# Performance work log

Measured on AMD Instinct MI355X. Metric: run time of the kernel, lower is better.

Reference implementation:

```python
import jax, jax.numpy as jnp
import numpy as np

N = 20000       # nodes
E = 320000      # edges (before self-loops)
F_IN = 128
HID = 128
HEADS = 4
OUT_DIM = 2
B = 64          # graphs in batch
SLOPE = 0.2     # GATv2 leaky_relu negative slope (PyG default)


def _glorot(key, shape):
    fan_in, fan_out = shape[0], shape[1]
    limit = np.sqrt(6.0 / (fan_in + fan_out)).astype(np.float32)
    return jax.random.uniform(key, shape, jnp.float32, -limit, limit)


def setup_inputs() -> dict:
    key = jax.random.key(0)
    ks = jax.random.split(key, 24)
    inp = {
        'x': jax.random.normal(ks[0], (N, F_IN), jnp.float32),
        'edge_src': jax.random.randint(ks[1], (E,), 0, N),
        'edge_dst': jax.random.randint(ks[2], (E,), 0, N),
        'batch': jnp.sort(jax.random.randint(ks[3], (N,), 0, B)),
        # layer 1: in=F_IN, out=HEADS*HID, concat
        'Wl1': _glorot(ks[4], (F_IN, HEADS * HID)),
        'Wr1': _glorot(ks[5], (F_IN, HEADS * HID)),
        'bl1': jnp.zeros((HEADS * HID,), jnp.float32),
        'br1': jnp.zeros((HEADS * HID,), jnp.float32),
        'att1': _glorot(ks[6], (HEADS, HID)),
        'bias1': jnp.zeros((HEADS * HID,), jnp.float32),
        # layer 2: in=HEADS*HID, out=HEADS*HID, concat
        'Wl2': _glorot(ks[7], (HEADS * HID, HEADS * HID)),
        'Wr2': _glorot(ks[8], (HEADS * HID, HEADS * HID)),
        'bl2': jnp.zeros((HEADS * HID,), jnp.float32),
        'br2': jnp.zeros((HEADS * HID,), jnp.float32),
        'att2': _glorot(ks[9], (HEADS, HID)),
        'bias2': jnp.zeros((HEADS * HID,), jnp.float32),
        # layer 3: in=HEADS*HID, heads=1, concat=False -> out=HID
        'Wl3': _glorot(ks[10], (HEADS * HID, HID)),
        'Wr3': _glorot(ks[11], (HEADS * HID, HID)),
        'bl3': jnp.zeros((HID,), jnp.float32),
        'br3': jnp.zeros((HID,), jnp.float32),
        'att3': _glorot(ks[12], (1, HID)),
        'bias3': jnp.zeros((HID,), jnp.float32),
        # output MLP
        'W_mlp1': _glorot(ks[13], (HID, HID)),
        'b_mlp1': jnp.zeros((HID,), jnp.float32),
        'W_mlp2': _glorot(ks[14], (HID, OUT_DIM)),
        'b_mlp2': jnp.zeros((OUT_DIM,), jnp.float32),
    }
    return inp


def gatv2_layer(x, src, dst, Wl, Wr, bl, br, att, bias, concat):
    """PyG GATv2Conv (eval mode): alpha_ij = softmax_j over N(i) of a^T LeakyReLU(xl_j + xr_i)."""
    H, C = att.shape
    n = x.shape[0]
    xl = (x @ Wl + bl).reshape(n, H, C)   # source transform
    e = jax.nn.leaky_relu(xl[src] + (x @ Wr + br).reshape(n, H, C)[dst], SLOPE)  # [E,H,C]
    logits = jnp.einsum('ehc,hc->eh', e, att)                                    # [E,H]
    # segment softmax over destination node
    m = jax.ops.segment_max(logits, dst, num_segments=n)
    alpha = jnp.exp(logits - m[dst])
    denom = jax.ops.segment_sum(alpha, dst, num_segments=n)
    alpha = alpha / denom[dst]
    out = jax.ops.segment_sum(xl[src] * alpha[..., None], dst, num_segments=n)   # [N,H,C]
    out = out.reshape(n, H * C) if concat else out.mean(axis=1)
    return out + bias


def reference(x, edge_src, edge_dst, batch,
              Wl1, Wr1, bl1, br1, att1, bias1,
              Wl2, Wr2, bl2, br2, att2, bias2,
              Wl3, Wr3, bl3, br3, att3, bias3,
              W_mlp1, b_mlp1, W_mlp2, b_mlp2):
    n = x.shape[0]
    loop = jnp.arange(n, dtype=edge_src.dtype)
    src = jnp.concatenate([edge_src, loop])   # PyG add_self_loops=True
    dst = jnp.concatenate([edge_dst, loop])

    h = jax.nn.elu(gatv2_layer(x, src, dst, Wl1, Wr1, bl1, br1, att1, bias1, True))
    h = jax.nn.elu(gatv2_layer(h, src, dst, Wl2, Wr2, bl2, br2, att2, bias2, True))
    h = jax.nn.elu(gatv2_layer(h, src, dst, Wl3, Wr3, bl3, br3, att3, bias3, False))

    # global_mean_pool over graph ids
    counts = jnp.maximum(jax.ops.segment_sum(jnp.ones((n,), h.dtype), batch, num_segments=B), 1.0)
    pooled = jax.ops.segment_sum(h, batch, num_segments=B) / counts[:, None]

    hidden = jax.nn.relu(pooled @ W_mlp1 + b_mlp1)
    return hidden @ W_mlp2 + b_mlp2
```

## Files before the change

### kernel.cpp

```cpp
#include <hip/hip_runtime.h>
#include <math.h>


typedef __attribute__((ext_vector_type(4))) float f32x4;
typedef __attribute__((ext_vector_type(8))) _Float16 f16x8;
typedef __attribute__((ext_vector_type(4))) _Float16 f16x4;
typedef __attribute__((ext_vector_type(2))) _Float16 f16x2;

__device__ __forceinline__ float elu1(float x) {
    return (x > 0.f) ? x : (__expf(x) - 1.f);
}
__device__ __forceinline__ f16x2 pk_leaky(f16x2 s) {
    const f16x2 slope = {(_Float16)0.2f, (_Float16)0.2f};
    return __builtin_elementwise_max(s, s * slope);
}

__device__ __forceinline__ float dpp_sum16(float v) {
    int t;
    t = __builtin_amdgcn_mov_dpp(__float_as_int(v), 0xB1, 0xF, 0xF, true);
    v += __int_as_float(t);
    t = __builtin_amdgcn_mov_dpp(__float_as_int(v), 0x4E, 0xF, 0xF, true);
    v += __int_as_float(t);
    t = __builtin_amdgcn_mov_dpp(__float_as_int(v), 0x141, 0xF, 0xF, true);
    v += __int_as_float(t);
    t = __builtin_amdgcn_mov_dpp(__float_as_int(v), 0x140, 0xF, 0xF, true);
    v += __int_as_float(t);
    return v;
}

__global__ void count_kernel(const int* __restrict__ dst, int* __restrict__ cnt,
                             int E, int N) {
    int e = blockIdx.x * 256 + threadIdx.x;
    if (e < E + N) {
        int d = (e < E) ? dst[e] : (e - E);
        atomicAdd(&cnt[d], 1);
    }
}

__global__ __launch_bounds__(256) void scan1_kernel(const int* __restrict__ cnt,
                                                    int* __restrict__ psum, int N) {
    __shared__ int red[256];
    int idx = blockIdx.x * 256 + threadIdx.x;
    red[threadIdx.x] = (idx < N) ? cnt[idx] : 0;
    __syncthreads();
    for (int s = 128; s > 0; s >>= 1) {
        if (threadIdx.x < s) red[threadIdx.x] += red[threadIdx.x + s];
        __syncthreads();
    }
    if (threadIdx.x == 0) psum[blockIdx.x] = red[0];
}
__global__ __launch_bounds__(128) void scan2_kernel(int* __restrict__ psum, int nch) {
    __shared__ int buf[128];
    int t = threadIdx.x;
    int v = (t < nch) ? psum[t] : 0;
    buf[t] = v;
    __syncthreads();
    for (int off = 1; off < 128; off <<= 1) {
        int x = (t >= off) ? buf[t - off] : 0;
        __syncthreads();
        buf[t] += x;
        __syncthreads();
    }
    if (t < nch) psum[t] = buf[t] - v;
}
__global__ __launch_bounds__(256) void scan3_kernel(const int* __restrict__ cnt,
                                                    const int* __restrict__ psum,
                                                    int* __restrict__ rowstart,
                                                    int* __restrict__ cursor, int N) {
    __shared__ int buf[256];
    int idx = blockIdx.x * 256 + threadIdx.x;
    int v = (idx < N) ? cnt[idx] : 0;
    buf[threadIdx.x] = v;
    __syncthreads();
    for (int off = 1; off < 256; off <<= 1) {
        int t = (threadIdx.x >= off) ? buf[threadIdx.x - off] : 0;
        __syncthreads();
        buf[threadIdx.x] += t;
        __syncthreads();
    }
    int excl = buf[threadIdx.x] - v + psum[blockIdx.x];
    if (idx < N) {
        rowstart[idx] = excl;
        cursor[idx]   = excl;
        if (idx == N - 1) rowstart[N] = excl + v;
    }
}

__global__ void scatter_kernel(const int* __restrict__ src, const int* __restrict__ dst,
                               int* __restrict__ cursor, int* __restrict__ csr_src,
                               int E, int N) {
    int e = blockIdx.x * 256 + threadIdx.x;
    if (e < E + N) {
        int d, s;
        if (e < E) { d = dst[e]; s = src[e]; }
        else       { d = e - E; s = e - E; }
        int pos = atomicAdd(&cursor[d], 1);
        csr_src[pos] = s;
    }
}

__device__ __forceinline__ void convWT_body(
    const float* __restrict__ Wl, const float* __restrict__ Wr,
    _Float16* __restrict__ Bth, _Float16* __restrict__ Btl,
    int K, int Nh, int bx, int by, int t) {
    __shared__ float tile[32][33];
    int kb = bx * 32;
    int nb = by * 32;
    int tx = t & 31;
    int ty = t >> 5;
#pragma unroll
    for (int j = 0; j < 4; ++j) {
        int kk = kb + ty + j * 8;
        int nn = nb + tx;
        float v = (nn < Nh) ? Wl[(size_t)kk * Nh + nn]
                            : Wr[(size_t)kk * Nh + (nn - Nh)];
        tile[ty + j * 8][tx] = v;
    }
    __syncthreads();
#pragma unroll
    for (int j = 0; j < 4; ++j) {
        int nn = nb + ty + j * 8;
        int kk = kb + tx;
        float v = tile[tx][ty + j * 8];
        _Float16 h = (_Float16)v;
        Bth[(size_t)nn * K + kk] = h;
        Btl[(size_t)nn * K + kk] = (_Float16)(v - (float)h);
    }
}

__global__ __launch_bounds__(256) void prep_kernel(
    const float* __restrict__ Wl1, const float* __restrict__ Wr1,
    _Float16* __restrict__ Wth1, _Float16* __restrict__ Wtl1,
    const float* __restrict__ Wl2, const float* __restrict__ Wr2,
    _Float16* __restrict__ Wth2, _Float16* __restrict__ Wtl2,
    const float* __restrict__ Wl3, const float* __restrict__ Wr3,
    _Float16* __restrict__ Wth3, _Float16* __restrict__ Wtl3,
    const float* __restrict__ X, _Float16* __restrict__ A,
    int n_valid, int n_total,
    const int* __restrict__ batch, int* __restrict__ gstart, int N, int B) {
    int b = blockIdx.x;
    int t = threadIdx.x;
    if (b < 128) {
        convWT_body(Wl1, Wr1, Wth1, Wtl1, 128, 512, b & 3, b >> 2, t);
    } else if (b < 640) {
        int l = b - 128;
        convWT_body(Wl2, Wr2, Wth2, Wtl2, 512, 512, l & 15, l >> 4, t);
    } else if (b < 768) {
        int l = b - 640;
        convWT_body(Wl3, Wr3, Wth3, Wtl3, 512, 128, l & 15, l >> 4, t);
    } else if (b < 3328) {
        int i = ((b - 768) * 256 + t) * 4;
        if (i < n_total) {
            float4 v = (i < n_valid) ? *(const float4*)(X + i)
                                     : make_float4(0.f, 0.f, 0.f, 0.f);
            f16x4 h;
            h.x = (_Float16)v.x; h.y = (_Float16)v.y;
            h.z = (_Float16)v.z; h.w = (_Float16)v.w;
            *(f16x4*)(A + i) = h;
        }
    } else {
        int n = (b - 3328) * 256 + t;
        if (n > N) return;
        int cur  = (n < N) ? batch[n] : B;
        int prev = (n == 0) ? -1 : batch[n - 1];
        for (int g = prev + 1; g <= cur; ++g) gstart[g] = n;
    }
}

#define SCW 132
__global__ __launch_bounds__(256, 1) void gemm_f16_kernel(
    const _Float16* __restrict__ A,
    const _Float16* __restrict__ Bh, const _Float16* __restrict__ Bl,
    const float* __restrict__ biasL, const float* __restrict__ biasR, int Nh_,
    _Float16* __restrict__ P, _Float16* __restrict__ Q, int K, int NT) {
    __shared__ __align__(16) char smem[49152];
    float* sC = (float*)(smem);

    const int tid  = threadIdx.x;
    const int lane = tid & 63;
    const int wv   = tid >> 6;
    const int wm   = wv & 1;
    const int wn   = wv >> 1;
    const int fm   = lane & 15;
    const int q    = lane >> 4;
    const int qa   = q ^ ((fm >> 1) & 3);

    const int bi = blockIdx.x;
    const int kx = bi & 7;
    const int tt = bi >> 3;
    const int m0 = ((tt / NT) * 8 + kx) * 128;
    const int n0 = (tt % NT) * 128;

    const int r0  = lane >> 2;
    const int kcs = (((lane & 3) ^ ((lane >> 3) & 3)) << 3);

    f32x4 acc[4][4];
#pragma unroll
    for (int i = 0; i < 4; ++i)
#pragma unroll
        for (int j = 0; j < 4; ++j) {
            acc[i][j].x = 0.f; acc[i][j].y = 0.f;
            acc[i][j].z = 0.f; acc[i][j].w = 0.f;
        }

    const int nIters = K >> 5;
    int cur = 0;
    {
        char* base = smem;
#pragma unroll
        for (int j = 0; j < 2; ++j) {
            int wc  = wv * 2 + j;
            int row = wc * 16 + r0;
            size_t ga = (size_t)(m0 + row) * K + kcs;
            size_t gb = (size_t)(n0 + row) * K + kcs;
            int lofs = wc * 1024;
            __builtin_amdgcn_global_load_lds(
                (const __attribute__((address_space(1))) void*)(A + ga),
                (__attribute__((address_space(3))) void*)(base + lofs), 16, 0, 0);
            __builtin_amdgcn_global_load_lds(
                (const __attribute__((address_space(1))) void*)(Bh + gb),
                (__attribute__((address_space(3))) void*)(base + 8192 + lofs), 16, 0, 0);
            __builtin_amdgcn_global_load_lds(
                (const __attribute__((address_space(1))) void*)(Bl + gb),
                (__attribute__((address_space(3))) void*)(base + 16384 + lofs), 16, 0, 0);
        }
    }
    for (int it = 0; it < nIters; ++it) {
        __syncthreads();
        if (it + 1 < nIters) {
            char* base = smem + (cur ^ 1) * 24576;
            int ks = (it + 1) << 5;
#pragma unroll
            for (int j = 0; j < 2; ++j) {
                int wc  = wv * 2 + j;
                int row = wc * 16 + r0;
                size_t ga = (size_t)(m0 + row) * K + ks + kcs;
                size_t gb = (size_t)(n0 + row) * K + ks + kcs;
                int lofs = wc * 1024;
                __builtin_amdgcn_global_load_lds(
                    (const __attribute__((address_space(1))) void*)(A + ga),
                    (__attribute__((address_space(3))) void*)(base + lofs), 16, 0, 0);
                __builtin_amdgcn_global_load_lds(
                    (const __attribute__((address_space(1))) void*)(Bh + gb),
                    (__attribute__((address_space(3))) void*)(base + 8192 + lofs), 16, 0, 0);
                __builtin_amdgcn_global_load_lds(
                    (const __attribute__((address_space(1))) void*)(Bl + gb),
                    (__attribute__((address_space(3))) void*)(base + 16384 + lofs), 16, 0, 0);
            }
        }

        _Float16* cA  = (_Float16*)(smem + cur * 24576);
        _Float16* cBh = (_Float16*)(smem + cur * 24576 + 8192);
        _Float16* cBl = (_Float16*)(smem + cur * 24576 + 16384);
        f16x8 ah[4];
#pragma unroll
        for (int mi = 0; mi < 4; ++mi)
            ah[mi] = *(const f16x8*)&cA[(wm * 64 + mi * 16 + fm) * 32 + qa * 8];
#pragma unroll
        for (int ni = 0; ni < 4; ++ni) {
            int r = (wn * 64 + ni * 16 + fm) * 32 + qa * 8;
            f16x8 bh = *(const f16x8*)&cBh[r];
            f16x8 bl = *(const f16x8*)&cBl[r];
#pragma unroll
            for (int mi = 0; mi < 4; ++mi) {
                acc[mi][ni] = __builtin_amdgcn_mfma_f32_16x16x32_f16(ah[mi], bh, acc[mi][ni], 0, 0, 0);
                acc[mi][ni] = __builtin_amdgcn_mfma_f32_16x16x32_f16(ah[mi], bl, acc[mi][ni], 0, 0, 0);
            }
        }
        cur ^= 1;
    }

    float bsv[4];
#pragma unroll
    for (int ni = 0; ni < 4; ++ni) {
        int col = n0 + wn * 64 + ni * 16 + fm;
        bsv[ni] = (col < Nh_) ? biasL[col] : biasR[col - Nh_];
    }

    _Float16* dstbase = (n0 < Nh_) ? P : Q;
    const int col0 = (n0 < Nh_) ? n0 : (n0 - Nh_);

#pragma unroll
    for (int c = 0; c < 2; ++c) {
        __syncthreads();
        if (wm == c) {
#pragma unroll
            for (int mi = 0; mi < 4; ++mi)
#pragma unroll
                for (int ni = 0; ni < 4; ++ni) {
                    int base = (mi * 16 + q * 4) * SCW + wn * 64 + ni * 16 + fm;
                    sC[base]           = acc[mi][ni].x + bsv[ni];
                    sC[base + SCW]     = acc[mi][ni].y + bsv[ni];
                    sC[base + 2 * SCW] = acc[mi][ni].z + bsv[ni];
                    sC[base + 3 * SCW] = acc[mi][ni].w + bsv[ni];
                }
        }
        __syncthreads();
#pragma unroll
        for (int j = 0; j < 8; ++j) {
            int flat = j * 256 + tid;
            int row  = flat >> 5;
            int col  = (flat & 31) * 4;
            f32x4 v = *(const f32x4*)(sC + row * SCW + col);
            f16x4 hv;
            hv.x = (_Float16)v.x; hv.y = (_Float16)v.y;
            hv.z = (_Float16)v.z; hv.w = (_Float16)v.w;
            *(f16x4*)(dstbase + (size_t)(m0 + c * 64 + row) * Nh_ + col0 + col) = hv;
        }
    }
}


__device__ __forceinline__ void edge4_one(
    int s, const _Float16* __restrict__ P, int c0,
    const f16x2* r2, const f16x2* t2, float& l_run, float* acc) {
    union { f16x8 v; f16x2 p[4]; } h;
    h.v = *(const f16x8*)(P + ((size_t)s << 9) + c0);
    float p = 0.f;
#pragma unroll
    for (int k = 0; k < 4; ++k)
        p = __builtin_amdgcn_fdot2(pk_leaky(h.p[k] + r2[k]), t2[k], p, false);
    p = dpp_sum16(p);
    float w = __expf(p);
    l_run += w;
#pragma unroll
    for (int j = 0; j < 8; ++j)
        acc[j] = fmaf((float)h.v[j], w, acc[j]);
}

__global__ __launch_bounds__(128) void gat_edge4_kernel(
    const _Float16* __restrict__ P, const _Float16* __restrict__ Q,
    const float* __restrict__ att, const float* __restrict__ bias,
    const int* __restrict__ rowstart, const int* __restrict__ srcs,
    _Float16* __restrict__ H, int N) {
    int wv = threadIdx.x >> 6;
    int lane = threadIdx.x & 63;
    int n = blockIdx.x * 2 + wv;
    if (n >= N) return;
    int c0 = lane * 8;

    f16x8 rv = *(const f16x8*)(Q + (size_t)n * 512 + c0);
    f16x2 r2[4], t2[4];
#pragma unroll
    for (int k = 0; k < 4; ++k) {
        r2[k].x = rv[2 * k]; r2[k].y = rv[2 * k + 1];
        t2[k].x = (_Float16)att[c0 + 2 * k];
        t2[k].y = (_Float16)att[c0 + 2 * k + 1];
    }

    float acc[8];
#pragma unroll
    for (int j = 0; j < 8; ++j) acc[j] = 0.f;
    float l_run = 0.f;

    int beg = __builtin_amdgcn_readfirstlane(rowstart[n]);
    int end = __builtin_amdgcn_readfirstlane(rowstart[n + 1]);

    int i = beg;
    int s0 = srcs[i], s1 = srcs[i + 1], s2 = srcs[i + 2], s3 = srcs[i + 3];

    for (; i + 3 < end; ) {
        int f0 = srcs[i + 4], f1 = srcs[i + 5], f2 = srcs[i + 6], f3 = srcs[i + 7];
        int u0 = __builtin_amdgcn_readfirstlane(s0);
        int u1 = __builtin_amdgcn_readfirstlane(s1);
        int u2 = __builtin_amdgcn_readfirstlane(s2);
        int u3 = __builtin_amdgcn_readfirstlane(s3);
        union { f16x8 v; f16x2 p[4]; } h0, h1, h2, h3;
        h0.v = *(const f16x8*)(P + ((size_t)u0 << 9) + c0);
        h1.v = *(const f16x8*)(P + ((size_t)u1 << 9) + c0);
        h2.v = *(const f16x8*)(P + ((size_t)u2 << 9) + c0);
        h3.v = *(const f16x8*)(P + ((size_t)u3 << 9) + c0);
        float p0 = 0.f, p1 = 0.f, p2 = 0.f, p3 = 0.f;
#pragma unroll
        for (int k = 0; k < 4; ++k) {
            p0 = __builtin_amdgcn_fdot2(pk_leaky(h0.p[k] + r2[k]), t2[k], p0, false);
            p1 = __builtin_amdgcn_fdot2(pk_leaky(h1.p[k] + r2[k]), t2[k], p1, false);
            p2 = __builtin_amdgcn_fdot2(pk_leaky(h2.p[k] + r2[k]), t2[k], p2, false);
            p3 = __builtin_amdgcn_fdot2(pk_leaky(h3.p[k] + r2[k]), t2[k], p3, false);
        }
        p0 = dpp_sum16(p0);
        p1 = dpp_sum16(p1);
        p2 = dpp_sum16(p2);
        p3 = dpp_sum16(p3);
        float w0 = __expf(p0);
        float w1 = __expf(p1);
        float w2 = __expf(p2);
        float w3 = __expf(p3);
        l_run += (w0 + w1) + (w2 + w3);
#pragma unroll
        for (int j = 0; j < 8; ++j) {
            float a = fmaf((float)h0.v[j], w0, acc[j]);
            a = fmaf((float)h1.v[j], w1, a);
            a = fmaf((float)h2.v[j], w2, a);
            acc[j] = fmaf((float)h3.v[j], w3, a);
        }
        i += 4; s0 = f0; s1 = f1; s2 = f2; s3 = f3;
    }
    int rem = end - i;
    if (rem > 0) edge4_one(__builtin_amdgcn_readfirstlane(s0), P, c0, r2, t2, l_run, acc);
    if (rem > 1) edge4_one(__builtin_amdgcn_readfirstlane(s1), P, c0, r2, t2, l_run, acc);
    if (rem > 2) edge4_one(__builtin_amdgcn_readfirstlane(s2), P, c0, r2, t2, l_run, acc);

    float inv = 1.f / l_run;
    f16x8 oh;
#pragma unroll
    for (int j = 0; j < 8; ++j)
        oh[j] = (_Float16)elu1(acc[j] * inv + bias[c0 + j]);
    *(f16x8*)(H + (size_t)n * 512 + c0) = oh;
}

__global__ __launch_bounds__(128) void gat_edge1_kernel(
    const _Float16* __restrict__ P, const _Float16* __restrict__ Q,
    const float* __restrict__ att, const float* __restrict__ bias,
    const int* __restrict__ rowstart, const int* __restrict__ srcs,
    float* __restrict__ out, int N) {
    int wv = threadIdx.x >> 6;
    int lane = threadIdx.x & 63;
    int n = blockIdx.x * 2 + wv;
    if (n >= N) return;
    int qd = lane >> 4;
    int lq = lane & 15;
    int c0 = lq * 8;

    f16x8 rv = *(const f16x8*)(Q + (size_t)n * 128 + c0);
    f16x2 r2[4], t2[4];
#pragma unroll
    for (int k = 0; k < 4; ++k) {
        r2[k].x = rv[2 * k]; r2[k].y = rv[2 * k + 1];
        t2[k].x = (_Float16)att[c0 + 2 * k];
        t2[k].y = (_Float16)att[c0 + 2 * k + 1];
    }

    float acc[8];
#pragma unroll
    for (int j = 0; j < 8; ++j) acc[j] = 0.f;
    float l_run = 0.f;

    int beg = __builtin_amdgcn_readfirstlane(rowstart[n]);
    int end = __builtin_amdgcn_readfirstlane(rowstart[n + 1]);
    for (int e = beg + qd; e < end; e += 4) {
        int s = srcs[e];
        union { f16x8 v; f16x2 p[4]; } hv;
        hv.v = *(const f16x8*)(P + ((size_t)s << 7) + c0);
        float p = 0.f;
#pragma unroll
        for (int k = 0; k < 4; ++k)
            p = __builtin_amdgcn_fdot2(pk_leaky(hv.p[k] + r2[k]), t2[k], p, false);
        p = dpp_sum16(p);
        float w = __expf(p);
        l_run += w;
#pragma unroll
        for (int j = 0; j < 8; ++j)
            acc[j] = fmaf((float)hv.v[j], w, acc[j]);
    }
    l_run += __shfl_xor(l_run, 16, 64);
    l_run += __shfl_xor(l_run, 32, 64);
#pragma unroll
    for (int j = 0; j < 8; ++j) {
        acc[j] += __shfl_xor(acc[j], 16, 64);
        acc[j] += __shfl_xor(acc[j], 32, 64);
    }
    float inv = 1.f / l_run;
    int cw = c0 + qd * 2;
    float2 w2;
    w2.x = elu1(acc[qd * 2]     * inv + bias[cw]);
    w2.y = elu1(acc[qd * 2 + 1] * inv + bias[cw + 1]);
    *(float2*)(out + (size_t)n * 128 + cw) = w2;
}

__global__ __launch_bounds__(256) void poolmlp_kernel(
    const float* __restrict__ h3, const int* __restrict__ gstart,
    const float* __restrict__ W1, const float* __restrict__ b1,
    const float* __restrict__ W2, const float* __restrict__ b2,
    float* __restrict__ out) {
    __shared__ float red[256];
    __shared__ float pr[128];
    __shared__ float2 mred[128];
    int g = blockIdx.x;
    int t = threadIdx.x;
    int c = t & 127;
    int h = t >> 7;
    int gs = gstart[g], ge = gstart[g + 1];
    float s = 0.f;
    for (int n = gs + h; n < ge; n += 2) s += h3[(size_t)n * 128 + c];
    red[t] = s;
    __syncthreads();
    if (h == 0) {
        float tot = red[c] + red[c + 128];
        float cntf = fmaxf((float)(ge - gs), 1.f);
        pr[c] = tot / cntf;
    }
    __syncthreads();
    if (t < 128) {
        float hh = b1[t];
#pragma unroll 4
        for (int k = 0; k < 128; ++k) hh = fmaf(pr[k], W1[k * 128 + t], hh);
        hh = fmaxf(hh, 0.0f);
        mred[t] = make_float2(hh * W2[t * 2], hh * W2[t * 2 + 1]);
    }
    __syncthreads();
    for (int ss = 64; ss > 0; ss >>= 1) {
        if (t < ss) {
            mred[t].x += mred[t + ss].x;
            mred[t].y += mred[t + ss].y;
        }
        __syncthreads();
    }
    if (t == 0) {
        out[g * 2]     = mred[0].x + b2[0];
        out[g * 2 + 1] = mred[0].y + b2[1];
    }
}

extern "C" void kernel_launch(void* const* d_in, const int* in_sizes, int n_in,
                              void* d_out, int out_size, void* d_ws, size_t ws_size,
                              hipStream_t stream) {
    const float* x     = (const float*)d_in[0];
    const int*   esrc  = (const int*)d_in[1];
    const int*   edst  = (const int*)d_in[2];
    const int*   batch = (const int*)d_in[3];
    const float* Wl1   = (const float*)d_in[4];
    const float* Wr1   = (const float*)d_in[5];
    const float* bl1   = (const float*)d_in[6];
    const float* br1   = (const float*)d_in[7];
    const float* att1  = (const float*)d_in[8];
    const float* bias1 = (const float*)d_in[9];
    const float* Wl2   = (const float*)d_in[10];
    const float* Wr2   = (const float*)d_in[11];
    const float* bl2   = (const float*)d_in[12];
    const float* br2   = (const float*)d_in[13];
    const float* att2  = (const float*)d_in[14];
    const float* bias2 = (const float*)d_in[15];
    const float* Wl3   = (const float*)d_in[16];
    const float* Wr3   = (const float*)d_in[17];
    const float* bl3   = (const float*)d_in[18];
    const float* br3   = (const float*)d_in[19];
    const float* att3  = (const float*)d_in[20];
    const float* bias3 = (const float*)d_in[21];
    const float* Wm1   = (const float*)d_in[22];
    const float* bm1   = (const float*)d_in[23];
    const float* Wm2   = (const float*)d_in[24];
    const float* bm2   = (const float*)d_in[25];

    int N  = in_sizes[0] / 128;
    int E  = in_sizes[1];
    int ET = E + N;
    int B  = out_size / 2;
    const int Mp = 160 * 128;
    int nch = (N + 255) / 256;

    char* ws = (char*)d_ws;
    size_t off = 0;
    auto alloc = [&](size_t bytes) -> void* {
        void* p = ws + off;
        off += (bytes + 255) & ~(size_t)255;
        return p;
    };
    _Float16* P    = (_Float16*)alloc((size_t)Mp * 512 * 2);
    _Float16* Q    = (_Float16*)alloc((size_t)Mp * 512 * 2);
    _Float16* A1   = (_Float16*)alloc((size_t)Mp * 128 * 2);
    _Float16* Hb   = (_Float16*)alloc((size_t)Mp * 512 * 2);
    _Float16* Wth1 = (_Float16*)alloc((size_t)1024 * 128 * 2);
    _Float16* Wtl1 = (_Float16*)alloc((size_t)1024 * 128 * 2);
    _Float16* Wth2 = (_Float16*)alloc((size_t)1024 * 512 * 2);
    _Float16* Wtl2 = (_Float16*)alloc((size_t)1024 * 512 * 2);
    _Float16* Wth3 = (_Float16*)alloc((size_t)256 * 512 * 2);
    _Float16* Wtl3 = (_Float16*)alloc((size_t)256 * 512 * 2);
    float*    R3   = (float*)alloc((size_t)Mp * 128 * 4);
    int*    cnt      = (int*)alloc((size_t)N * 4);
    int*    psum     = (int*)alloc((size_t)(nch + 1) * 4);
    int*    rowstart = (int*)alloc((size_t)(N + 1) * 4);
    int*    cursor   = (int*)alloc((size_t)N * 4);
    int*    csr_src  = (int*)alloc((size_t)ET * 4 + 64);
    int*    gstart   = (int*)alloc((size_t)(B + 1) * 4);
    (void)ws_size;

    hipMemsetAsync(cnt, 0, (size_t)N * 4, stream);

    count_kernel<<<(ET + 255) / 256, 256, 0, stream>>>(edst, cnt, E, N);
    scan1_kernel<<<nch, 256, 0, stream>>>(cnt, psum, N);
    scan2_kernel<<<1, 128, 0, stream>>>(psum, nch);
    scan3_kernel<<<nch, 256, 0, stream>>>(cnt, psum, rowstart, cursor, N);
    scatter_kernel<<<(ET + 255) / 256, 256, 0, stream>>>(esrc, edst, cursor, csr_src, E, N);

    prep_kernel<<<3407, 256, 0, stream>>>(
        Wl1, Wr1, Wth1, Wtl1, Wl2, Wr2, Wth2, Wtl2, Wl3, Wr3, Wth3, Wtl3,
        x, A1, N * 128, Mp * 128, batch, gstart, N, B);

    int eblocks = (N + 1) / 2;

    gemm_f16_kernel<<<160 * 8, 256, 0, stream>>>(A1, Wth1, Wtl1, bl1, br1, 512, P, Q, 128, 8);
    gat_edge4_kernel<<<eblocks, 128, 0, stream>>>(P, Q, att1, bias1, rowstart, csr_src, Hb, N);

    gemm_f16_kernel<<<160 * 8, 256, 0, stream>>>(Hb, Wth2, Wtl2, bl2, br2, 512, P, Q, 512, 8);
    gat_edge4_kernel<<<eblocks, 128, 0, stream>>>(P, Q, att2, bias2, rowstart, csr_src, Hb, N);

    gemm_f16_kernel<<<160 * 2, 256, 0, stream>>>(Hb, Wth3, Wtl3, bl3, br3, 128, P, Q, 512, 2);
    gat_edge1_kernel<<<eblocks, 128, 0, stream>>>(P, Q, att3, bias3, rowstart, csr_src, R3, N);

    poolmlp_kernel<<<B, 256, 0, stream>>>(R3, gstart, Wm1, bm1, Wm2, bm2, (float*)d_out);
}
```

Before: 396.3 us.

## Load GEMM B operands directly from global into registers; fuse count into prep

The GEMM kernel no longer stages the weight hi/lo tiles in LDS. Each wave now loads its B fragments straight from global memory (relying on L2/L1 caching of the small weight matrices), which shrinks shared memory from 48KB to 34KB and cuts the LDS staging traffic. Separately, the edge-count atomic kernel is folded into the prep kernel as extra blocks, saving one launch. The risk is global-load latency in the inner loop, since B loads are no longer prefetched asynchronously, plus uncoalesced row-strided accesses.

```diff
diff --git a/kernel.cpp b/kernel.cpp
--- a/kernel.cpp
+++ b/kernel.cpp
@@ -28,15 +28,6 @@
     return v;
 }
 
-__global__ void count_kernel(const int* __restrict__ dst, int* __restrict__ cnt,
-                             int E, int N) {
-    int e = blockIdx.x * 256 + threadIdx.x;
-    if (e < E + N) {
-        int d = (e < E) ? dst[e] : (e - E);
-        atomicAdd(&cnt[d], 1);
-    }
-}
-
 __global__ __launch_bounds__(256) void scan1_kernel(const int* __restrict__ cnt,
                                                     int* __restrict__ psum, int N) {
     __shared__ int red[256];
@@ -137,7 +128,8 @@
     _Float16* __restrict__ Wth3, _Float16* __restrict__ Wtl3,
     const float* __restrict__ X, _Float16* __restrict__ A,
     int n_valid, int n_total,
-    const int* __restrict__ batch, int* __restrict__ gstart, int N, int B) {
+    const int* __restrict__ batch, int* __restrict__ gstart, int N, int B,
+    const int* __restrict__ edst, int* __restrict__ cnt, int E) {
     int b = blockIdx.x;
     int t = threadIdx.x;
     if (b < 128) {
@@ -158,12 +150,18 @@
             h.z = (_Float16)v.z; h.w = (_Float16)v.w;
             *(f16x4*)(A + i) = h;
         }
-    } else {
+    } else if (b < 3407) {
         int n = (b - 3328) * 256 + t;
         if (n > N) return;
         int cur  = (n < N) ? batch[n] : B;
         int prev = (n == 0) ? -1 : batch[n - 1];
         for (int g = prev + 1; g <= cur; ++g) gstart[g] = n;
+    } else {
+        int e = (b - 3407) * 256 + t;
+        if (e < E + N) {
+            int d = (e < E) ? edst[e] : (e - E);
+            atomicAdd(&cnt[d], 1);
+        }
     }
 }
 
@@ -173,7 +171,7 @@
     const _Float16* __restrict__ Bh, const _Float16* __restrict__ Bl,
     const float* __restrict__ biasL, const float* __restrict__ biasR, int Nh_,
     _Float16* __restrict__ P, _Float16* __restrict__ Q, int K, int NT) {
-    __shared__ __align__(16) char smem[49152];
+    __shared__ __align__(16) char smem[34816];
     float* sC = (float*)(smem);
 
     const int tid  = threadIdx.x;
@@ -212,59 +210,46 @@
             int wc  = wv * 2 + j;
             int row = wc * 16 + r0;
             size_t ga = (size_t)(m0 + row) * K + kcs;
-            size_t gb = (size_t)(n0 + row) * K + kcs;
             int lofs = wc * 1024;
             __builtin_amdgcn_global_load_lds(
                 (const __attribute__((address_space(1))) void*)(A + ga),
                 (__attribute__((address_space(3))) void*)(base + lofs), 16, 0, 0);
-            __builtin_amdgcn_global_load_lds(
-                (const __attribute__((address_space(1))) void*)(Bh + gb),
-                (__attribute__((address_space(3))) void*)(base + 8192 + lofs), 16, 0, 0);
-            __builtin_amdgcn_global_load_lds(
-                (const __attribute__((address_space(1))) void*)(Bl + gb),
-                (__attribute__((address_space(3))) void*)(base + 16384 + lofs), 16, 0, 0);
-        }
-    }
+        }
+    }
+    const int brow = n0 + wn * 64 + fm;
     for (int it = 0; it < nIters; ++it) {
         __syncthreads();
         if (it + 1 < nIters) {
-            char* base = smem + (cur ^ 1) * 24576;
-            int ks = (it + 1) << 5;
+            char* base = smem + (cur ^ 1) * 8192;
+            int ks2 = (it + 1) << 5;
 #pragma unroll
             for (int j = 0; j < 2; ++j) {
                 int wc  = wv * 2 + j;
                 int row = wc * 16 + r0;
-                size_t ga = (size_t)(m0 + row) * K + ks + kcs;
-                size_t gb = (size_t)(n0 + row) * K + ks + kcs;
+                size_t ga = (size_t)(m0 + row) * K + ks2 + kcs;
                 int lofs = wc * 1024;
                 __builtin_amdgcn_global_load_lds(
                     (const __attribute__((address_space(1))) void*)(A + ga),
                     (__attribute__((address_space(3))) void*)(base + lofs), 16, 0, 0);
-                __builtin_amdgcn_global_load_lds(
-                    (const __attribute__((address_space(1))) void*)(Bh + gb),
-                    (__attribute__((address_space(3))) void*)(base + 8192 + lofs), 16, 0, 0);
-                __builtin_amdgcn_global_load_lds(
-                    (const __attribute__((address_space(1))) void*)(Bl + gb),
-                    (__attribute__((address_space(3))) void*)(base + 16384 + lofs), 16, 0, 0);
             }
         }
-
-        _Float16* cA  = (_Float16*)(smem + cur * 24576);
-        _Float16* cBh = (_Float16*)(smem + cur * 24576 + 8192);
-        _Float16* cBl = (_Float16*)(smem + cur * 24576 + 16384);
+        int ks = it << 5;
+        f16x8 bhv[4];
+#pragma unroll
+        for (int ni = 0; ni < 4; ++ni)
+            bhv[ni] = *(const f16x8*)(Bh + (size_t)(brow + ni * 16) * K + ks + q * 8);
+        _Float16* cA = (_Float16*)(smem + cur * 8192);
         f16x8 ah[4];
 #pragma unroll
         for (int mi = 0; mi < 4; ++mi)
             ah[mi] = *(const f16x8*)&cA[(wm * 64 + mi * 16 + fm) * 32 + qa * 8];
 #pragma unroll
         for (int ni = 0; ni < 4; ++ni) {
-            int r = (wn * 64 + ni * 16 + fm) * 32 + qa * 8;
-            f16x8 bh = *(const f16x8*)&cBh[r];
-            f16x8 bl = *(const f16x8*)&cBl[r];
+            f16x8 blv = *(const f16x8*)(Bl + (size_t)(brow + ni * 16) * K + ks + q * 8);
 #pragma unroll
             for (int mi = 0; mi < 4; ++mi) {
-                acc[mi][ni] = __builtin_amdgcn_mfma_f32_16x16x32_f16(ah[mi], bh, acc[mi][ni], 0, 0, 0);
-                acc[mi][ni] = __builtin_amdgcn_mfma_f32_16x16x32_f16(ah[mi], bl, acc[mi][ni], 0, 0, 0);
+                acc[mi][ni] = __builtin_amdgcn_mfma_f32_16x16x32_f16(ah[mi], bhv[ni], acc[mi][ni], 0, 0, 0);
+                acc[mi][ni] = __builtin_amdgcn_mfma_f32_16x16x32_f16(ah[mi], blv, acc[mi][ni], 0, 0, 0);
             }
         }
         cur ^= 1;
@@ -577,15 +562,15 @@
 
     hipMemsetAsync(cnt, 0, (size_t)N * 4, stream);
 
-    count_kernel<<<(ET + 255) / 256, 256, 0, stream>>>(edst, cnt, E, N);
+    int cblocks = (ET + 255) / 256;
+    prep_kernel<<<3407 + cblocks, 256, 0, stream>>>(
+        Wl1, Wr1, Wth1, Wtl1, Wl2, Wr2, Wth2, Wtl2, Wl3, Wr3, Wth3, Wtl3,
+        x, A1, N * 128, Mp * 128, batch, gstart, N, B, edst, cnt, E);
+
     scan1_kernel<<<nch, 256, 0, stream>>>(cnt, psum, N);
     scan2_kernel<<<1, 128, 0, stream>>>(psum, nch);
     scan3_kernel<<<nch, 256, 0, stream>>>(cnt, psum, rowstart, cursor, N);
-    scatter_kernel<<<(ET + 255) / 256, 256, 0, stream>>>(esrc, edst, cursor, csr_src, E, N);
-
-    prep_kernel<<<3407, 256, 0, stream>>>(
-        Wl1, Wr1, Wth1, Wtl1, Wl2, Wr2, Wth2, Wtl2, Wl3, Wr3, Wth3, Wtl3,
-        x, A1, N * 128, Mp * 128, batch, gstart, N, B);
+    scatter_kernel<<<cblocks, 256, 0, stream>>>(esrc, edst, cursor, csr_src, E, N);
 
     int eblocks = (N + 1) / 2;
 
```

After: 457.4 us. 1.15x slower.
